# Optimization experiments

Measured on AMD Instinct MI355X. Metric: run time of the kernel, lower is better.

The kernel has to match this reference:

```python
import jax, jax.numpy as jnp
import numpy as np
from jax import lax

B, S, DM = 4, 4096, 1024
H, P, R = 16, 32, 8
D = DM // H  # head_dim = 64
K_SEL = 4


def setup_inputs() -> dict:
    key = jax.random.key(0)
    ks = jax.random.split(key, 6)
    x = jax.random.normal(ks[0], (B, S, DM), dtype=jnp.float32)
    K_state = jax.random.normal(ks[1], (H, P, R, D), dtype=jnp.float32) / np.sqrt(D)
    V_state = jax.random.normal(ks[2], (H, P, R, D), dtype=jnp.float32) / np.sqrt(D)
    W_router = jax.random.normal(ks[3], (H, D, P), dtype=jnp.float32) / np.sqrt(D)
    W_out = jax.random.normal(ks[4], (DM, DM), dtype=jnp.float32) / np.sqrt(DM)
    b_out = jnp.zeros((DM,), dtype=jnp.float32)
    return {"x": x, "K_state": K_state, "V_state": V_state,
            "W_router": W_router, "W_out": W_out, "b_out": b_out, "k": K_SEL}


def reference(x, K_state, V_state, W_router, W_out, b_out, k):
    b, s, dm = x.shape
    h, p, r, d = K_state.shape
    xh = x.reshape(b, s, h, d)  # per-head token features

    # Router: top-k partition selection per token per head.
    logits = jnp.einsum('bshd,hdp->bshp', xh, W_router)
    topv = lax.top_k(logits, k)[0]            # [b,s,h,k]
    thresh = topv[..., -1:]                   # k-th largest logit
    neg_inf = jnp.array(-jnp.inf, dtype=logits.dtype)
    gates = jax.nn.softmax(jnp.where(logits >= thresh, logits, neg_inf), axis=-1)  # [b,s,h,p], zero off top-k

    # Attention over state rows within each partition (masked-dense == sparse gather math).
    scale = jnp.asarray(1.0 / np.sqrt(d), dtype=x.dtype)
    scores = jnp.einsum('bshd,hprd->bshpr', xh, K_state) * scale
    attn = jax.nn.softmax(scores, axis=-1)    # softmax over rows r within a partition

    # Gate-weighted combine of per-partition attention outputs, fused to avoid [b,s,h,p,d].
    w = attn * gates[..., None]               # [b,s,h,p,r]
    heads = jnp.einsum('bshpr,hprd->bshd', w, V_state)

    out = heads.reshape(b, s, dm) @ W_out + b_out
    return out
```

## Files before the change

### kernel.cpp

```cpp
#include <hip/hip_runtime.h>
#include <hip/hip_bf16.h>

#define BB 4
#define SS 4096
#define DM 1024
#define HH 16
#define PP 32
#define RR 8
#define DD 64
#define NTOK (BB*SS)
#define MM NTOK
#define NN DM
#define KK DM

typedef __attribute__((ext_vector_type(8))) short short8;
typedef __attribute__((ext_vector_type(4))) float floatx4;

static __device__ inline short f2bf(float f) {
    union { __hip_bfloat16 b; short s; } u; u.b = __float2bfloat16(f); return u.s;
}
static __device__ inline short8 pack8(float4 lo, float4 hi) {
    short8 r;
    r[0] = f2bf(lo.x); r[1] = f2bf(lo.y); r[2] = f2bf(lo.z); r[3] = f2bf(lo.w);
    r[4] = f2bf(hi.x); r[5] = f2bf(hi.y); r[6] = f2bf(hi.z); r[7] = f2bf(hi.w);
    return r;
}

static __device__ inline unsigned bfr(float f) {
    unsigned u = __float_as_uint(f);
    return u + 0x7fffu + ((u >> 16) & 1u);
}
static __device__ inline int pk2(float a, float b) {
    return __builtin_amdgcn_perm(bfr(b), bfr(a), 0x07060302);
}
static __device__ inline short8 pk8(float4 lo, float4 hi) {
    union { short8 s; int i[4]; } r;
    r.i[0] = pk2(lo.x, lo.y); r.i[1] = pk2(lo.z, lo.w);
    r.i[2] = pk2(hi.x, hi.y); r.i[3] = pk2(hi.z, hi.w);
    return r.s;
}

__global__ __launch_bounds__(256) void convert_w(const float* __restrict__ Wo,
                                                 __hip_bfloat16* __restrict__ wsw) {
    int tid = blockIdx.x * 256 + threadIdx.x;
    int l = tid & 63;
    int kblk = (tid >> 6) & 31;
    int ntile = tid >> 11;
    int col = ntile * 16 + (l & 15);
    int krow = kblk * 32 + (l >> 4) * 8;
#pragma unroll
    for (int j = 0; j < 8; ++j) {
        wsw[(size_t)tid * 8 + j] = __float2bfloat16(Wo[(size_t)(krow + j) * NN + col]);
    }
}

__global__ __launch_bounds__(256) void convert_kv(const float* __restrict__ Kst,
                                                  const float* __restrict__ Vst,
                                                  __hip_bfloat16* __restrict__ kfrag,
                                                  __hip_bfloat16* __restrict__ vfrag) {
    int tid = blockIdx.x * 256 + threadIdx.x;
    int arr = tid >> 15;
    int idx = tid & 32767;
    int h = idx >> 11, blk = (idx >> 6) & 31, fl = idx & 63;
    int fm = fl & 15, fk = fl >> 4;
    short8 val;
    short* dst;
    if (arr == 0) {
        int mt = blk >> 1, kb = blk & 1;
        int pr = mt * 16 + fm, d0 = kb * 32 + fk * 8;
        const float* src = Kst + ((size_t)h * 256 + pr) * 64 + d0;
        float4 lo = *(const float4*)src, hi = *(const float4*)(src + 4);
        val = pack8(lo, hi);
        dst = (short*)kfrag + (size_t)idx * 8;
    } else {
        int mt = blk >> 3, kb = blk & 7;
        int d = mt * 16 + fm, pr0 = kb * 32 + fk * 8;
        const float* src = Vst + ((size_t)h * 256 + pr0) * 64 + d;
#pragma unroll
        for (int j = 0; j < 8; ++j) val[j] = f2bf(src[j * 64]);
        dst = (short*)vfrag + (size_t)idx * 8;
    }
    *(short8*)dst = val;
}

__global__ __launch_bounds__(256, 3) void attn_v4(const float* __restrict__ x,
                                                  const float* __restrict__ Wr,
                                                  const __hip_bfloat16* __restrict__ kfrag,
                                                  const __hip_bfloat16* __restrict__ vfrag,
                                                  const int* __restrict__ kp,
                                                  __hip_bfloat16* __restrict__ hb) {
    __shared__ __align__(16) char smem[41984];
    float (*xs)[68]    = (float (*)[68])smem;
    float (*Lg)[36]    = (float (*)[36])(smem + 17408);
    short* wf          = (short*)smem;
    float (*gates)[36] = (float (*)[36])(smem + 32768);

    const int lane = threadIdx.x & 63;
    const int w = threadIdx.x >> 6;
    const int l15 = lane & 15, l4 = lane >> 4;
    const int t0 = blockIdx.x * 64;
    const int h = blockIdx.y;

    {
        int row = threadIdx.x >> 2, q = threadIdx.x & 3;
        const float4* src = (const float4*)(x + (size_t)(t0 + row) * DM + h * 64 + q * 16);
        float4 v0 = src[0], v1 = src[1], v2 = src[2], v3 = src[3];
        float4* dst = (float4*)&xs[row][q * 16];
        dst[0] = v0; dst[1] = v1; dst[2] = v2; dst[3] = v3;
    }

    const int p = lane & 31, dh = lane >> 5;
    float wreg[32];
    {
        const float* wrp = Wr + (size_t)h * (DD * PP) + dh * 32 * PP + p;
#pragma unroll
        for (int dd = 0; dd < 32; ++dd) wreg[dd] = wrp[dd * PP];
    }
    const int kkv = kp[0];

    __syncthreads();

    short8 xb[4][2];
#pragma unroll
    for (int nt = 0; nt < 4; ++nt)
#pragma unroll
        for (int kb = 0; kb < 2; ++kb) {
            const float* bp = x + (size_t)(t0 + nt * 16 + l15) * DM + h * 64 + kb * 32 + l4 * 8;
            float4 lo = *(const float4*)bp;
            float4 hi = *(const float4*)(bp + 4);
            xb[nt][kb] = pk8(lo, hi);
        }
    short8 ka[4][2];
#pragma unroll
    for (int mi = 0; mi < 4; ++mi)
#pragma unroll
        for (int kb = 0; kb < 2; ++kb)
            ka[mi][kb] = *(const short8*)((const short*)kfrag +
                          ((size_t)(h * 32 + (w * 4 + mi) * 2 + kb) * 512 + lane * 8));

    floatx4 acc[4][4] = {};
#pragma unroll
    for (int kb = 0; kb < 2; ++kb)
#pragma unroll
        for (int mi = 0; mi < 4; ++mi)
#pragma unroll
            for (int nt = 0; nt < 4; ++nt)
                acc[mi][nt] = __builtin_amdgcn_mfma_f32_16x16x32_bf16(ka[mi][kb], xb[nt][kb], acc[mi][nt], 0, 0, 0);

    for (int it = 0; it < 16; ++it) {
        int t = w * 16 + it;
        float xf[32];
#pragma unroll
        for (int j = 0; j < 8; ++j) {
            float4 tq = *(const float4*)&xs[t][dh * 32 + 4 * j];
            xf[4 * j] = tq.x; xf[4 * j + 1] = tq.y; xf[4 * j + 2] = tq.z; xf[4 * j + 3] = tq.w;
        }
        float lg = 0.f;
#pragma unroll
        for (int dd = 0; dd < 32; ++dd) lg += xf[dd] * wreg[dd];
        lg += __shfl_xor(lg, 32);
        if (lane < 32) Lg[t][lane] = lg;
    }
    __syncthreads();

    if (lane < 16) {
        int t = w * 16 + lane;
        float lgr[32];
        const float4* lrow = (const float4*)&Lg[t][0];
#pragma unroll
        for (int c = 0; c < 8; ++c) {
            float4 q4 = lrow[c];
            lgr[4 * c] = q4.x; lgr[4 * c + 1] = q4.y; lgr[4 * c + 2] = q4.z; lgr[4 * c + 3] = q4.w;
        }
        float a1 = -INFINITY, b2 = -INFINITY, c3 = -INFINITY, d4 = -INFINITY;
#pragma unroll
        for (int pp = 0; pp < 32; ++pp) {
            float v = lgr[pp];
            float na = fmaxf(a1, v); v = fminf(a1, v); a1 = na;
            float nb = fmaxf(b2, v); v = fminf(b2, v); b2 = nb;
            float nc = fmaxf(c3, v); v = fminf(c3, v); c3 = nc;
            d4 = fmaxf(d4, v);
        }
        float thresh = (kkv >= 4) ? d4 : (kkv == 3 ? c3 : (kkv == 2 ? b2 : a1));
        float den = 0.f;
        float garr[32];
#pragma unroll
        for (int pp = 0; pp < 32; ++pp) {
            float e = __expf(lgr[pp] - a1);
            float ge = (lgr[pp] >= thresh) ? e : 0.f;
            garr[pp] = ge; den += ge;
        }
        float inv = 1.f / den;
        float4* grow = (float4*)&gates[t][0];
#pragma unroll
        for (int c = 0; c < 8; ++c)
            grow[c] = make_float4(garr[4 * c] * inv, garr[4 * c + 1] * inv,
                                  garr[4 * c + 2] * inv, garr[4 * c + 3] * inv);
    }
    __syncthreads();

#pragma unroll
    for (int mi = 0; mi < 4; ++mi) {
        const int mt = w * 4 + mi;
        const int pidx = mt * 2 + (l4 >> 1);
#pragma unroll
        for (int nt = 0; nt < 4; ++nt) {
            float g = gates[nt * 16 + l15][pidx];
            float s0 = acc[mi][nt][0] * 0.125f;
            float s1 = acc[mi][nt][1] * 0.125f;
            float s2 = acc[mi][nt][2] * 0.125f;
            float s3 = acc[mi][nt][3] * 0.125f;
            float mx = fmaxf(fmaxf(s0, s1), fmaxf(s2, s3));
            mx = fmaxf(mx, __shfl_xor(mx, 16));
            float e0 = __expf(s0 - mx), e1 = __expf(s1 - mx);
            float e2 = __expf(s2 - mx), e3 = __expf(s3 - mx);
            float loc = (e0 + e1) + (e2 + e3);
            float se = loc + __shfl_xor(loc, 16);
            float ws = g / se;
            int2 pk;
            pk.x = pk2(e0 * ws, e1 * ws);
            pk.y = pk2(e2 * ws, e3 * ws);
            int off = (((mt & 1) * 2 + (l4 >> 1)) * 16 + l15) * 8 + (l4 & 1) * 4;
            *(int2*)&wf[(nt * 8 + (mt >> 1)) * 512 + off] = pk;
        }
    }
    __syncthreads();

    floatx4 h4[4] = {};
#pragma unroll
    for (int kb = 0; kb < 8; ++kb) {
        short8 va = *(const short8*)((const short*)vfrag +
                      ((size_t)(h * 32 + w * 8 + kb) * 512 + lane * 8));
#pragma unroll
        for (int nt = 0; nt < 4; ++nt) {
            short8 wb = *(const short8*)&wf[(nt * 8 + kb) * 512 + lane * 8];
            h4[nt] = __builtin_amdgcn_mfma_f32_16x16x32_bf16(va, wb, h4[nt], 0, 0, 0);
        }
    }
#pragma unroll
    for (int nt = 0; nt < 4; ++nt) {
        int t = t0 + nt * 16 + l15;
        int2 pk;
        pk.x = pk2(h4[nt][0], h4[nt][1]);
        pk.y = pk2(h4[nt][2], h4[nt][3]);
        *(int2*)((short*)hb + (size_t)t * DM + h * 64 + w * 16 + l4 * 4) = pk;
    }
}

__global__ __launch_bounds__(256) void gemm_v2(const __hip_bfloat16* __restrict__ Abf,
                                               const __hip_bfloat16* __restrict__ Bsw,
                                               const float* __restrict__ bias,
                                               float* __restrict__ C) {
    __shared__ __align__(16) short As[4096];
    const int lane = threadIdx.x & 63;
    const int wave = threadIdx.x >> 6;
    const int wm = wave >> 1, wn = wave & 1;
    const int bm0 = blockIdx.y * 128;
    const int bn0 = blockIdx.x * 128;
    const int l15 = lane & 15, l4 = lane >> 4;

    const short* Ap = (const short*)Abf;
    const short* Bp = (const short*)Bsw;

    const int c0 = (wave * 2 + 0) * 64 + lane;
    const int c1 = (wave * 2 + 1) * 64 + lane;
    const short* g0 = Ap + (size_t)(bm0 + (c0 >> 2)) * KK + (c0 & 3) * 8;
    const short* g1 = Ap + (size_t)(bm0 + (c1 >> 2)) * KK + (c1 & 3) * 8;
    short* l0 = &As[(wave * 2 + 0) * 512];
    short* l1 = &As[(wave * 2 + 1) * 512];

    int boff[4];
#pragma unroll
    for (int nt = 0; nt < 4; ++nt)
        boff[nt] = (((bn0 >> 4) + wn * 4 + nt) * 32) * 512 + lane * 8;

    int aoff[4];
#pragma unroll
    for (int mt = 0; mt < 4; ++mt)
        aoff[mt] = ((wm * 64 + mt * 16 + l15) * 4 + l4) * 8;

    floatx4 acc[4][4] = {};

    for (int kb = 0; kb < 32; ++kb) {
        __syncthreads();
        short8 b[4];
#pragma unroll
        for (int nt = 0; nt < 4; ++nt)
            b[nt] = *(const short8*)(Bp + boff[nt] + kb * 512);
        __builtin_amdgcn_global_load_lds(
            (const __attribute__((address_space(1))) unsigned int*)(g0 + kb * 32),
            (__attribute__((address_space(3))) unsigned int*)l0, 16, 0, 0);
        __builtin_amdgcn_global_load_lds(
            (const __attribute__((address_space(1))) unsigned int*)(g1 + kb * 32),
            (__attribute__((address_space(3))) unsigned int*)l1, 16, 0, 0);
        __syncthreads();
        short8 a[4];
#pragma unroll
        for (int mt = 0; mt < 4; ++mt)
            a[mt] = *(const short8*)&As[aoff[mt]];
#pragma unroll
        for (int mt = 0; mt < 4; ++mt)
#pragma unroll
            for (int nt = 0; nt < 4; ++nt)
                acc[mt][nt] = __builtin_amdgcn_mfma_f32_16x16x32_bf16(a[mt], b[nt], acc[mt][nt], 0, 0, 0);
    }

#pragma unroll
    for (int nt = 0; nt < 4; ++nt) {
        const int col = bn0 + wn * 64 + nt * 16 + l15;
        const float bv = bias[col];
#pragma unroll
        for (int mt = 0; mt < 4; ++mt) {
            const int row0 = bm0 + wm * 64 + mt * 16 + l4 * 4;
#pragma unroll
            for (int i = 0; i < 4; ++i)
                C[(size_t)(row0 + i) * NN + col] = acc[mt][nt][i] + bv;
        }
    }
}

extern "C" void kernel_launch(void* const* d_in, const int* in_sizes, int n_in,
                              void* d_out, int out_size, void* d_ws, size_t ws_size,
                              hipStream_t stream) {
    const float* x   = (const float*)d_in[0];
    const float* Kst = (const float*)d_in[1];
    const float* Vst = (const float*)d_in[2];
    const float* Wr  = (const float*)d_in[3];
    const float* Wo  = (const float*)d_in[4];
    const float* bo  = (const float*)d_in[5];
    const int*   kp  = (const int*)d_in[6];
    float* out = (float*)d_out;

    __hip_bfloat16* hb    = (__hip_bfloat16*)d_ws;
    __hip_bfloat16* wsw   = hb + (size_t)MM * KK;
    __hip_bfloat16* kfrag = wsw + (size_t)KK * NN;
    __hip_bfloat16* vfrag = kfrag + 16 * 32 * 512;

    convert_w<<<dim3(512), 256, 0, stream>>>(Wo, wsw);
    convert_kv<<<dim3(256), 256, 0, stream>>>(Kst, Vst, kfrag, vfrag);
    attn_v4<<<dim3(NTOK / 64, HH), 256, 0, stream>>>(x, Wr, kfrag, vfrag, kp, hb);
    gemm_v2<<<dim3(NN / 128, MM / 128), 256, 0, stream>>>(hb, wsw, bo, out);
}
```

Baseline: 264.1 us.

## Split router into its own kernel and pass gates through global memory

```diff
diff --git a/kernel.cpp b/kernel.cpp
--- a/kernel.cpp
+++ b/kernel.cpp
@@ -83,21 +83,15 @@
     *(short8*)dst = val;
 }
 
-__global__ __launch_bounds__(256, 3) void attn_v4(const float* __restrict__ x,
-                                                  const float* __restrict__ Wr,
-                                                  const __hip_bfloat16* __restrict__ kfrag,
-                                                  const __hip_bfloat16* __restrict__ vfrag,
-                                                  const int* __restrict__ kp,
-                                                  __hip_bfloat16* __restrict__ hb) {
-    __shared__ __align__(16) char smem[41984];
-    float (*xs)[68]    = (float (*)[68])smem;
-    float (*Lg)[36]    = (float (*)[36])(smem + 17408);
-    short* wf          = (short*)smem;
-    float (*gates)[36] = (float (*)[36])(smem + 32768);
+__global__ __launch_bounds__(256, 4) void router(const float* __restrict__ x,
+                                                 const float* __restrict__ Wr,
+                                                 const int* __restrict__ kp,
+                                                 float* __restrict__ gates_g) {
+    __shared__ __align__(16) float xs[64][68];
+    __shared__ __align__(16) float Lg[64][36];
 
     const int lane = threadIdx.x & 63;
     const int w = threadIdx.x >> 6;
-    const int l15 = lane & 15, l4 = lane >> 4;
     const int t0 = blockIdx.x * 64;
     const int h = blockIdx.y;
 
@@ -120,33 +114,6 @@
 
     __syncthreads();
 
-    short8 xb[4][2];
-#pragma unroll
-    for (int nt = 0; nt < 4; ++nt)
-#pragma unroll
-        for (int kb = 0; kb < 2; ++kb) {
-            const float* bp = x + (size_t)(t0 + nt * 16 + l15) * DM + h * 64 + kb * 32 + l4 * 8;
-            float4 lo = *(const float4*)bp;
-            float4 hi = *(const float4*)(bp + 4);
-            xb[nt][kb] = pk8(lo, hi);
-        }
-    short8 ka[4][2];
-#pragma unroll
-    for (int mi = 0; mi < 4; ++mi)
-#pragma unroll
-        for (int kb = 0; kb < 2; ++kb)
-            ka[mi][kb] = *(const short8*)((const short*)kfrag +
-                          ((size_t)(h * 32 + (w * 4 + mi) * 2 + kb) * 512 + lane * 8));
-
-    floatx4 acc[4][4] = {};
-#pragma unroll
-    for (int kb = 0; kb < 2; ++kb)
-#pragma unroll
-        for (int mi = 0; mi < 4; ++mi)
-#pragma unroll
-            for (int nt = 0; nt < 4; ++nt)
-                acc[mi][nt] = __builtin_amdgcn_mfma_f32_16x16x32_bf16(ka[mi][kb], xb[nt][kb], acc[mi][nt], 0, 0, 0);
-
     for (int it = 0; it < 16; ++it) {
         int t = w * 16 + it;
         float xf[32];
@@ -191,12 +158,66 @@
             garr[pp] = ge; den += ge;
         }
         float inv = 1.f / den;
-        float4* grow = (float4*)&gates[t][0];
+        float4* grow = (float4*)&gates_g[((size_t)h * NTOK + t0 + t) * 32];
 #pragma unroll
         for (int c = 0; c < 8; ++c)
             grow[c] = make_float4(garr[4 * c] * inv, garr[4 * c + 1] * inv,
                                   garr[4 * c + 2] * inv, garr[4 * c + 3] * inv);
     }
+}
+
+__global__ __launch_bounds__(256, 3) void attn_v5(const float* __restrict__ x,
+                                                  const __hip_bfloat16* __restrict__ kfrag,
+                                                  const __hip_bfloat16* __restrict__ vfrag,
+                                                  const float* __restrict__ gates_g,
+                                                  __hip_bfloat16* __restrict__ hb) {
+    __shared__ __align__(16) float gates[64][36];
+    __shared__ __align__(16) short wf[16384];
+
+    const int lane = threadIdx.x & 63;
+    const int w = threadIdx.x >> 6;
+    const int l15 = lane & 15, l4 = lane >> 4;
+    const int t0 = blockIdx.x * 64;
+    const int h = blockIdx.y;
+
+    {
+        int j0 = threadIdx.x * 2;
+#pragma unroll
+        for (int u = 0; u < 2; ++u) {
+            int j = j0 + u;
+            int t = j >> 3, c = j & 7;
+            float4 g4 = *(const float4*)&gates_g[((size_t)h * NTOK + t0 + t) * 32 + c * 4];
+            *(float4*)&gates[t][c * 4] = g4;
+        }
+    }
+
+    short8 xb[4][2];
+#pragma unroll
+    for (int nt = 0; nt < 4; ++nt)
+#pragma unroll
+        for (int kb = 0; kb < 2; ++kb) {
+            const float* bp = x + (size_t)(t0 + nt * 16 + l15) * DM + h * 64 + kb * 32 + l4 * 8;
+            float4 lo = *(const float4*)bp;
+            float4 hi = *(const float4*)(bp + 4);
+            xb[nt][kb] = pk8(lo, hi);
+        }
+    short8 ka[4][2];
+#pragma unroll
+    for (int mi = 0; mi < 4; ++mi)
+#pragma unroll
+        for (int kb = 0; kb < 2; ++kb)
+            ka[mi][kb] = *(const short8*)((const short*)kfrag +
+                          ((size_t)(h * 32 + (w * 4 + mi) * 2 + kb) * 512 + lane * 8));
+
+    floatx4 acc[4][4] = {};
+#pragma unroll
+    for (int kb = 0; kb < 2; ++kb)
+#pragma unroll
+        for (int mi = 0; mi < 4; ++mi)
+#pragma unroll
+            for (int nt = 0; nt < 4; ++nt)
+                acc[mi][nt] = __builtin_amdgcn_mfma_f32_16x16x32_bf16(ka[mi][kb], xb[nt][kb], acc[mi][nt], 0, 0, 0);
+
     __syncthreads();
 
 #pragma unroll
@@ -229,21 +250,24 @@
     floatx4 h4[4] = {};
 #pragma unroll
     for (int kb = 0; kb < 8; ++kb) {
-        short8 va = *(const short8*)((const short*)vfrag +
-                      ((size_t)(h * 32 + w * 8 + kb) * 512 + lane * 8));
-#pragma unroll
-        for (int nt = 0; nt < 4; ++nt) {
-            short8 wb = *(const short8*)&wf[(nt * 8 + kb) * 512 + lane * 8];
-            h4[nt] = __builtin_amdgcn_mfma_f32_16x16x32_bf16(va, wb, h4[nt], 0, 0, 0);
-        }
-    }
-#pragma unroll
-    for (int nt = 0; nt < 4; ++nt) {
-        int t = t0 + nt * 16 + l15;
-        int2 pk;
-        pk.x = pk2(h4[nt][0], h4[nt][1]);
-        pk.y = pk2(h4[nt][2], h4[nt][3]);
-        *(int2*)((short*)hb + (size_t)t * DM + h * 64 + w * 16 + l4 * 4) = pk;
+        short8 wb = *(const short8*)&wf[(w * 8 + kb) * 512 + lane * 8];
+#pragma unroll
+        for (int mt = 0; mt < 4; ++mt) {
+            short8 va = *(const short8*)((const short*)vfrag +
+                          ((size_t)(h * 32 + mt * 8 + kb) * 512 + lane * 8));
+            h4[mt] = __builtin_amdgcn_mfma_f32_16x16x32_bf16(va, wb, h4[mt], 0, 0, 0);
+        }
+    }
+    {
+        const int t = t0 + w * 16 + l15;
+        short* dstbase = (short*)hb + (size_t)t * DM + h * 64;
+#pragma unroll
+        for (int mt = 0; mt < 4; ++mt) {
+            int2 pk;
+            pk.x = pk2(h4[mt][0], h4[mt][1]);
+            pk.y = pk2(h4[mt][2], h4[mt][3]);
+            *(int2*)(dstbase + mt * 16 + l4 * 4) = pk;
+        }
     }
 }
 
@@ -335,9 +359,11 @@
     __hip_bfloat16* wsw   = hb + (size_t)MM * KK;
     __hip_bfloat16* kfrag = wsw + (size_t)KK * NN;
     __hip_bfloat16* vfrag = kfrag + 16 * 32 * 512;
+    float* gates_g = out;
 
     convert_w<<<dim3(512), 256, 0, stream>>>(Wo, wsw);
     convert_kv<<<dim3(256), 256, 0, stream>>>(Kst, Vst, kfrag, vfrag);
-    attn_v4<<<dim3(NTOK / 64, HH), 256, 0, stream>>>(x, Wr, kfrag, vfrag, kp, hb);
+    router<<<dim3(NTOK / 64, HH), 256, 0, stream>>>(x, Wr, kp, gates_g);
+    attn_v5<<<dim3(NTOK / 64, HH), 256, 0, stream>>>(x, kfrag, vfrag, gates_g, hb);
     gemm_v2<<<dim3(NN / 128, MM / 128), 256, 0, stream>>>(hb, wsw, bo, out);
 }
```

Result: slower. 273.2 us (+3.4%).
